# Kernel optimization log

Hardware: AMD Instinct MI355X
Metric: run time of the kernel (lower is better)

The kernel has to match this reference:

```python
import jax, jax.numpy as jnp
import numpy as np

N_NODES = 100000
N_EDGES = 3200000
N_FEAT = 128
DIM = 256
N_CLASSES = 16
BN_EPS = 1e-5


def _glorot(key, shape):
    fan_in, fan_out = shape[0], shape[1]
    lim = float(np.sqrt(6.0 / (fan_in + fan_out)))
    return jax.random.uniform(key, shape, jnp.float32, -lim, lim)


def setup_inputs() -> dict:
    key = jax.random.key(0)
    ks = jax.random.split(key, 16)
    x = jax.random.normal(ks[0], (N_NODES, N_FEAT), jnp.float32)
    edge_index = jax.random.randint(ks[1], (2, N_EDGES), 0, N_NODES, jnp.int64)
    inp = {"x": x, "edge_index": edge_index}
    # conv1 MLP: num_features -> dim -> dim
    inp["w1a"] = _glorot(ks[2], (N_FEAT, DIM)); inp["b1a"] = jnp.zeros((DIM,), jnp.float32)
    inp["w1b"] = _glorot(ks[3], (DIM, DIM));    inp["b1b"] = jnp.zeros((DIM,), jnp.float32)
    inp["g1"] = jnp.ones((DIM,), jnp.float32);  inp["be1"] = jnp.zeros((DIM,), jnp.float32)
    # conv2 MLP
    inp["w2a"] = _glorot(ks[4], (DIM, DIM)); inp["b2a"] = jnp.zeros((DIM,), jnp.float32)
    inp["w2b"] = _glorot(ks[5], (DIM, DIM)); inp["b2b"] = jnp.zeros((DIM,), jnp.float32)
    inp["g2"] = jnp.ones((DIM,), jnp.float32); inp["be2"] = jnp.zeros((DIM,), jnp.float32)
    # conv3 MLP
    inp["w3a"] = _glorot(ks[6], (DIM, DIM)); inp["b3a"] = jnp.zeros((DIM,), jnp.float32)
    inp["w3b"] = _glorot(ks[7], (DIM, DIM)); inp["b3b"] = jnp.zeros((DIM,), jnp.float32)
    # fc2: dim -> num_classes
    inp["wfc"] = _glorot(ks[8], (DIM, N_CLASSES)); inp["bfc"] = jnp.zeros((N_CLASSES,), jnp.float32)
    return inp


def _gin_conv(h, src, dst, wa, ba, wb, bb):
    # sum-aggregate neighbor features: agg[i] = sum_{(j->i)} h[j]; eps=0 so root weight = 1
    agg = jax.ops.segment_sum(h[src], dst, num_segments=N_NODES)
    z = jax.nn.relu((h + agg) @ wa + ba)
    return z @ wb + bb


def _batchnorm(h, gamma, beta):
    # training-mode BN over node dim (biased variance, as torch forward)
    m = h.mean(axis=0)
    v = ((h - m) ** 2).mean(axis=0)
    return gamma * (h - m) / jnp.sqrt(v + BN_EPS) + beta


def reference(x, edge_index, w1a, b1a, w1b, b1b, g1, be1,
              w2a, b2a, w2b, b2b, g2, be2,
              w3a, b3a, w3b, b3b, wfc, bfc):
    src, dst = edge_index[0], edge_index[1]
    h = jax.nn.relu(_gin_conv(x, src, dst, w1a, b1a, w1b, b1b))
    h = _batchnorm(h, g1, be1)
    h = jax.nn.relu(_gin_conv(h, src, dst, w2a, b2a, w2b, b2b))
    h = _batchnorm(h, g2, be2)
    h = jax.nn.relu(_gin_conv(h, src, dst, w3a, b3a, w3b, b3b))
    # dropout p=0.5 is identity in eval mode
    logits = h @ wfc + bfc
    return jax.nn.log_softmax(logits, axis=-1)
```

## Files before the change

### kernel.cpp

```cpp
#include <hip/hip_runtime.h>

typedef unsigned int  u32;
typedef unsigned short u16;

#define NND 100000
#define MPAD 100096
#define NE  3200000
#define F0  128
#define DIM 256
#define NC  16

#define BSH   9
#define NBUCK 196
#define CAP   18432
#define EPB   8192

typedef __bf16 bf16x8 __attribute__((ext_vector_type(8)));
typedef float  f32x4  __attribute__((ext_vector_type(4)));

__device__ __forceinline__ float b2f(u16 h){ return __uint_as_float(((u32)h)<<16); }
__device__ __forceinline__ u16 f2b(float f){
    u32 u = __float_as_uint(f);
    return (u16)((u + 0x7fffu + ((u>>16)&1u)) >> 16);
}
__device__ __forceinline__ float lo16(u32 u){ return __uint_as_float(u<<16); }
__device__ __forceinline__ float hi16(u32 u){ return __uint_as_float(u & 0xffff0000u); }

__device__ __forceinline__ void gload16(const u16* g, u16* l){
    __builtin_amdgcn_global_load_lds(
        (const __attribute__((address_space(1))) u32*)g,
        (__attribute__((address_space(3))) u32*)l, 16, 0, 0);
}

__global__ void probe_kernel(const u32* __restrict__ xw, const int* __restrict__ ei,
                             int* __restrict__ mode, int* __restrict__ gcur,
                             float* __restrict__ stats){
    int t = threadIdx.x;
    if(t < NBUCK) gcur[t] = 0;
    #pragma unroll
    for(int i=0;i<4;i++) stats[t + 256*i] = 0.f;
    if(t==0){
        int insane = 0;
        for(int i=0;i<64;i++){
            u32 w  = xw[i];
            u32 lo = w & 0xffffu;
            u32 e  = (lo >> 7) & 0xff;
            if(lo != 0 && (e < 48 || e > 208)) insane++;
        }
        mode[0] = (insane > 8) ? 1 : 0;
        int zeros = 0;
        for(int i=0;i<16;i++) if(ei[2*i+1]==0) zeros++;
        mode[1] = (zeros==16) ? 1 : 0;
    }
}

__device__ __forceinline__ int ld_src(const int* ei, int i64f, long e){
    return i64f ? ei[2*e] : ei[e];
}
__device__ __forceinline__ int ld_dst(const int* ei, int i64f, long e){
    return i64f ? ei[2*((long)NE + e)] : ei[(long)NE + e];
}

__global__ __launch_bounds__(256) void bucketA(const int* __restrict__ ei,
        const int* __restrict__ mode, u32* __restrict__ bucketArr,
        int* __restrict__ gcur){
    __shared__ u32 stag[EPB];
    __shared__ u16 sbuck[EPB];
    __shared__ int cnt[NBUCK];
    __shared__ int ofs[NBUCK];
    __shared__ int wofs[NBUCK];
    __shared__ int gbase[NBUCK];
    __shared__ int ps[256];
    int tid = threadIdx.x;
    int i64f = mode[1];
    long e0 = (long)blockIdx.x * EPB;
    int n = (int)min((long)EPB, (long)NE - e0);
    if(tid < NBUCK) cnt[tid] = 0;
    __syncthreads();
    for(int i=tid;i<n;i+=256){
        int d = ld_dst(ei, i64f, e0+i);
        atomicAdd(&cnt[d>>BSH], 1);
    }
    __syncthreads();
    ps[tid] = (tid < NBUCK) ? cnt[tid] : 0;
    __syncthreads();
    for(int o=1;o<256;o<<=1){
        int v = (tid>=o) ? ps[tid-o] : 0;
        __syncthreads();
        ps[tid] += v;
        __syncthreads();
    }
    if(tid < NBUCK){
        int ex = ps[tid] - cnt[tid];
        ofs[tid] = ex; wofs[tid] = ex;
        gbase[tid] = cnt[tid] ? atomicAdd(&gcur[tid], cnt[tid]) : 0;
    }
    __syncthreads();
    for(int i=tid;i<n;i+=256){
        int s = ld_src(ei, i64f, e0+i);
        int d = ld_dst(ei, i64f, e0+i);
        int b = d>>BSH;
        int r = atomicAdd(&wofs[b], 1);
        stag[r]  = ((u32)s<<BSH) | (u32)(d & ((1<<BSH)-1));
        sbuck[r] = (u16)b;
    }
    __syncthreads();
    for(int i=tid;i<n;i+=256){
        int b = sbuck[i];
        int pos = gbase[b] + (i - ofs[b]);
        if(pos < CAP) bucketArr[(size_t)b*CAP + pos] = stag[i];
    }
}

__global__ __launch_bounds__(256) void bucketB(const u32* __restrict__ bucketArr,
        const int* __restrict__ gcnt,
        int* __restrict__ rp, int* __restrict__ ssrc){
    __shared__ u32 stag[CAP];
    __shared__ int deg[512];
    __shared__ int lrp[512];
    __shared__ int cur[512];
    __shared__ int ps[256];
    int b = blockIdx.x, tid = threadIdx.x;
    ps[tid] = (tid < NBUCK) ? gcnt[tid] : 0;
    __syncthreads();
    for(int o=1;o<256;o<<=1){
        int v = (tid>=o) ? ps[tid-o] : 0;
        __syncthreads();
        ps[tid] += v;
        __syncthreads();
    }
    int base = (b>0) ? ps[b-1] : 0;
    int n = min(gcnt[b], CAP);
    const u32* ba = bucketArr + (size_t)b*CAP;
    deg[tid] = 0; deg[tid+256] = 0;
    __syncthreads();
    for(int i=tid;i<n;i+=256){
        atomicAdd(&deg[ba[i] & 511], 1);
    }
    __syncthreads();
    ps[tid] = deg[2*tid] + deg[2*tid+1];
    __syncthreads();
    for(int o=1;o<256;o<<=1){
        int v = (tid>=o) ? ps[tid-o] : 0;
        __syncthreads();
        ps[tid] += v;
        __syncthreads();
    }
    {
        int ep = (tid==0) ? 0 : ps[tid-1];
        lrp[2*tid]   = ep;
        lrp[2*tid+1] = ep + deg[2*tid];
        cur[2*tid]   = lrp[2*tid];
        cur[2*tid+1] = lrp[2*tid+1];
    }
    __syncthreads();
    for(int i=tid;i<512;i+=256){
        int node = (b<<BSH) + i;
        if(node <= NND) rp[node] = base + lrp[i];
    }
    for(int i=tid;i<n;i+=256){
        u32 v = ba[i];
        int r = atomicAdd(&cur[v & 511], 1);
        stag[r] = v >> BSH;
    }
    __syncthreads();
    for(int i=tid;i<n;i+=256){
        ssrc[base + i] = (int)stag[i];
    }
}

__global__ void cvt_x(const float* __restrict__ xf, u16* __restrict__ Xc,
                      const int* __restrict__ mode){
    if(!mode[0]) return;
    size_t i = ((size_t)blockIdx.x*256 + threadIdx.x)*8;
    float4 a = *(const float4*)(xf+i);
    float4 b = *(const float4*)(xf+i+4);
    uint4 pk;
    pk.x = (u32)f2b(a.x) | ((u32)f2b(a.y)<<16);
    pk.y = (u32)f2b(a.z) | ((u32)f2b(a.w)<<16);
    pk.z = (u32)f2b(b.x) | ((u32)f2b(b.y)<<16);
    pk.w = (u32)f2b(b.z) | ((u32)f2b(b.w)<<16);
    *(uint4*)(Xc + i) = pk;
}

__device__ __forceinline__ float ldf(const void* p, int i, int f32f){
    return f32f ? ((const float*)p)[i] : b2f(((const u16*)p)[i]);
}
__global__ void merged_cvt(
        const void* w1a, const void* w1b, const void* w2a, const void* w2b,
        const void* w3a, const void* w3b, const void* wfc,
        const void* b1a, const void* b1b, const void* g1, const void* be1,
        const void* b2a, const void* b2b, const void* g2, const void* be2,
        const void* b3a, const void* b3b, const void* bfcp,
        u16* __restrict__ Wt1a, u16* __restrict__ Wt1b, u16* __restrict__ Wt2a,
        u16* __restrict__ Wt2b, u16* __restrict__ Wt3a, u16* __restrict__ Wt3b,
        u16* __restrict__ Wfc, u16* __restrict__ Vc, const int* __restrict__ mode){
    int b = blockIdx.x, t = threadIdx.x;
    int f32f = mode[0];
    if(b < 128){
        int id = b*256 + t;
        int k = id / DIM, n = id % DIM;
        Wt1a[n*F0 + k] = f2b(ldf(w1a, id, f32f));
        return;
    }
    b -= 128;
    if(b < 5*256){
        int wi = b >> 8;
        const void* W = (wi==0)?w1b:(wi==1)?w2a:(wi==2)?w2b:(wi==3)?w3a:w3b;
        u16* Wt = (wi==0)?Wt1b:(wi==1)?Wt2a:(wi==2)?Wt2b:(wi==3)?Wt3a:Wt3b;
        int id = (b & 255)*256 + t;
        int k = id / DIM, n = id % DIM;
        Wt[n*DIM + k] = f2b(ldf(W, id, f32f));
        return;
    }
    b -= 5*256;
    if(b < 16){
        int id = b*256 + t;
        int k = id / NC, c = id % NC;
        Wfc[c*DIM + k] = f2b(ldf(wfc, id, f32f));
        return;
    }
    b -= 16;
    {
        const void* ps[11] = {b1a,b1b,g1,be1,b2a,b2b,g2,be2,b3a,b3b,bfcp};
        int lens[11] = {DIM,DIM,DIM,DIM,DIM,DIM,DIM,DIM,DIM,DIM,NC};
        if(t < lens[b]) Vc[b*256 + t] = f2b(ldf(ps[b], t, f32f));
    }
}

template<int LPI>
__global__ __launch_bounds__(256) void agg2(const u16* __restrict__ hA,
        const u16* __restrict__ hB, const int* __restrict__ mode,
        const int* __restrict__ rp, const int* __restrict__ ssrc,
        u16* __restrict__ out,
        const float* __restrict__ stats, const u16* __restrict__ g,
        const u16* __restrict__ be, int use_bn, int M){
    const int F = LPI*8;
    const int IPW = 64/LPI;
    int node = blockIdx.x*4 + (threadIdx.x>>6);
    if(node >= M) return;
    int lane = threadIdx.x & 63;
    int li   = lane & (LPI-1);
    int slot = lane / LPI;
    const u16* h = (LPI==16 && mode[0]) ? hB : hA;
    const int boff = li*8;

    int e0 = rp[node], e1 = rp[node+1];
    int n_items = e1 - e0 + 1;
    float acc[8] = {0.f,0.f,0.f,0.f,0.f,0.f,0.f,0.f};

    auto item = [&](int i)->int { return (i==0) ? node : ssrc[e0 + i - 1]; };
    auto addu = [&](uint4 u){
        acc[0]+=lo16(u.x); acc[1]+=hi16(u.x);
        acc[2]+=lo16(u.y); acc[3]+=hi16(u.y);
        acc[4]+=lo16(u.z); acc[5]+=hi16(u.z);
        acc[6]+=lo16(u.w); acc[7]+=hi16(u.w);
    };

    int i = 0;
    for(; i + 4*IPW <= n_items; i += 4*IPW){
        int s0 = item(i + slot);
        int s1 = item(i + IPW + slot);
        int s2 = item(i + 2*IPW + slot);
        int s3 = item(i + 3*IPW + slot);
        uint4 u0 = *(const uint4*)(h + (size_t)s0*F + boff);
        uint4 u1 = *(const uint4*)(h + (size_t)s1*F + boff);
        uint4 u2 = *(const uint4*)(h + (size_t)s2*F + boff);
        uint4 u3 = *(const uint4*)(h + (size_t)s3*F + boff);
        addu(u0); addu(u1); addu(u2); addu(u3);
    }
    for(; i + IPW <= n_items; i += IPW){
        int s = item(i + slot);
        addu(*(const uint4*)(h + (size_t)s*F + boff));
    }
    if(i < n_items){
        int r = n_items - i;
        if(slot < r){
            int s = item(i + slot);
            addu(*(const uint4*)(h + (size_t)s*F + boff));
        }
    }

    #pragma unroll
    for(int j=0;j<8;j++){
        if(LPI==16) acc[j] += __shfl_xor(acc[j], 16);
        acc[j] += __shfl_xor(acc[j], 32);
    }

    if(slot == 0){
        float res[8];
        if(use_bn){
            float inv_m = 1.0f / (float)M;
            float cnt = (float)n_items;
            #pragma unroll
            for(int j=0;j<8;j++){
                int f = boff + j;
                float mean = stats[f]*inv_m;
                float var  = fmaxf(stats[F+f]*inv_m - mean*mean, 0.f);
                float rstd = rsqrtf(var + 1e-5f);
                float gg = b2f(g[f]);
                float a = gg*rstd;
                float bb = b2f(be[f]) - a*mean;
                res[j] = a*acc[j] + cnt*bb;
            }
        } else {
            #pragma unroll
            for(int j=0;j<8;j++) res[j] = acc[j];
        }
        uint4 o;
        o.x = (u32)f2b(res[0]) | ((u32)f2b(res[1])<<16);
        o.y = (u32)f2b(res[2]) | ((u32)f2b(res[3])<<16);
        o.z = (u32)f2b(res[4]) | ((u32)f2b(res[5])<<16);
        o.w = (u32)f2b(res[6]) | ((u32)f2b(res[7])<<16);
        *(uint4*)(out + (size_t)node*F + boff) = o;
    }
}

#define TBM 128
#define TBN 128
#define TBK 32
__global__ __launch_bounds__(256) void gemm128(
        const u16* __restrict__ A, const u16* __restrict__ Bt,
        const u16* __restrict__ bias, u16* __restrict__ C,
        int N, int K, int do_relu, float* __restrict__ stats, int do_stats){
    __shared__ __align__(16) u16 lA[TBM*TBK];
    __shared__ __align__(16) u16 lB[TBN*TBK];
    __shared__ float colS[TBN], colS2[TBN];
    int tid = threadIdx.x;
    int w = tid>>6, lane = tid&63;
    int q = lane>>4, mr = lane&15;
    int wr = w>>1, wc = w&1;
    int m0 = blockIdx.x*TBM, n0 = blockIdx.y*TBN;

    if(do_stats){
        if(tid < TBN){ colS[tid]=0.f; colS2[tid]=0.f; }
    }

    f32x4 acc[4][4];
    #pragma unroll
    for(int i=0;i<4;i++)
        #pragma unroll
        for(int c=0;c<4;c++) acc[i][c] = (f32x4){0.f,0.f,0.f,0.f};

    const u16* ga0 = A  + (size_t)(m0 + w*32 + (lane>>2))*K + (lane&3)*8;
    const u16* ga1 = ga0 + (size_t)16*K;
    const u16* gb0 = Bt + (size_t)(n0 + w*32 + (lane>>2))*K + (lane&3)*8;
    const u16* gb1 = gb0 + (size_t)16*K;
    u16* la0 = &lA[(w*32)*TBK];    u16* la1 = la0 + 16*TBK;
    u16* lb0 = &lB[(w*32)*TBK];    u16* lb1 = lb0 + 16*TBK;

    for(int k0=0; k0<K; k0+=TBK){
        gload16(ga0, la0); gload16(ga1, la1);
        gload16(gb0, lb0); gload16(gb1, lb1);
        ga0 += TBK; ga1 += TBK; gb0 += TBK; gb1 += TBK;
        __syncthreads();
        bf16x8 af[4], bfr[4];
        #pragma unroll
        for(int i=0;i<4;i++)
            af[i] = *reinterpret_cast<const bf16x8*>(&lA[(wr*64 + i*16 + mr)*TBK + q*8]);
        #pragma unroll
        for(int c=0;c<4;c++)
            bfr[c] = *reinterpret_cast<const bf16x8*>(&lB[(wc*64 + c*16 + mr)*TBK + q*8]);
        #pragma unroll
        for(int i=0;i<4;i++)
            #pragma unroll
            for(int c=0;c<4;c++)
                acc[i][c] = __builtin_amdgcn_mfma_f32_16x16x32_bf16(af[i], bfr[c], acc[i][c], 0, 0, 0);
        __syncthreads();
    }

    #pragma unroll
    for(int c=0;c<4;c++){
        int lcol = wc*64 + c*16 + mr;
        int col  = n0 + lcol;
        float bv = b2f(bias[col]);
        float s = 0.f, s2 = 0.f;
        #pragma unroll
        for(int i=0;i<4;i++){
            int row = m0 + wr*64 + i*16 + q*4;
            #pragma unroll
            for(int r=0;r<4;r++){
                float v = acc[i][c][r] + bv;
                if(do_relu) v = fmaxf(v, 0.f);
                u16 o = f2b(v);
                C[(size_t)(row + r)*N + col] = o;
                if(do_stats && (row + r) < NND){
                    float vr = b2f(o);
                    s += vr; s2 += vr*vr;
                }
            }
        }
        if(do_stats){
            atomicAdd(&colS[lcol], s);
            atomicAdd(&colS2[lcol], s2);
        }
    }
    if(do_stats){
        __syncthreads();
        if(tid < TBN){
            int col = n0 + tid;
            atomicAdd(&stats[col], colS[tid]);
            atomicAdd(&stats[DIM+col], colS2[tid]);
        }
    }
}

__global__ __launch_bounds__(256) void fc_lsm(const u16* __restrict__ h,
        const u16* __restrict__ wfcT, const u16* __restrict__ bfc,
        void* __restrict__ out, const int* __restrict__ mode, int M){
    __shared__ float lds[256];
    __shared__ float rmx[16], rls[16];
    int tid = threadIdx.x;
    int r = tid>>4, c = tid&15;
    int row = blockIdx.x*16 + r;
    float acc = b2f(bfc[c]);
    const u16* hp = h + (size_t)row*DIM;
    const u16* wp = wfcT + c*DIM;
    for(int k=0;k<DIM;k+=8){
        uint4 hv = *(const uint4*)(hp+k);
        uint4 wv = *(const uint4*)(wp+k);
        acc += lo16(hv.x)*lo16(wv.x) + hi16(hv.x)*hi16(wv.x)
             + lo16(hv.y)*lo16(wv.y) + hi16(hv.y)*hi16(wv.y)
             + lo16(hv.z)*lo16(wv.z) + hi16(hv.z)*hi16(wv.z)
             + lo16(hv.w)*lo16(wv.w) + hi16(hv.w)*hi16(wv.w);
    }
    lds[tid] = acc;
    __syncthreads();
    if(c==0){
        float mx = -1e30f;
        for(int i=0;i<NC;i++) mx = fmaxf(mx, lds[r*NC+i]);
        float s = 0.f;
        for(int i=0;i<NC;i++) s += expf(lds[r*NC+i] - mx);
        rmx[r] = mx; rls[r] = logf(s);
    }
    __syncthreads();
    if(row < M){
        float v = acc - rmx[r] - rls[r];
        if(mode[0]) ((float*)out)[(size_t)row*NC + c] = v;
        else        ((u16*)out)[(size_t)row*NC + c] = f2b(v);
    }
}

extern "C" void kernel_launch(void* const* d_in, const int* in_sizes, int n_in,
                              void* d_out, int out_size, void* d_ws, size_t ws_size,
                              hipStream_t stream){
    const void* x   = d_in[0];
    const int*  ei  = (const int*)d_in[1];
    const void* w1a = d_in[2];  const void* b1a = d_in[3];
    const void* w1b = d_in[4];  const void* b1b = d_in[5];
    const void* g1  = d_in[6];  const void* be1 = d_in[7];
    const void* w2a = d_in[8];  const void* b2a = d_in[9];
    const void* w2b = d_in[10]; const void* b2b = d_in[11];
    const void* g2  = d_in[12]; const void* be2 = d_in[13];
    const void* w3a = d_in[14]; const void* b3a = d_in[15];
    const void* w3b = d_in[16]; const void* b3b = d_in[17];
    const void* wfc = d_in[18]; const void* bfc = d_in[19];

    char* base = (char*)d_ws;
    size_t off = 0;
    auto alloc = [&](size_t bytes)->void*{
        void* p = base + off;
        off = (off + bytes + 255) & ~(size_t)255;
        return p;
    };
    u16*  P     = (u16*)alloc((size_t)MPAD*DIM*2);
    u16*  Q     = (u16*)alloc((size_t)MPAD*DIM*2);
    int*  ssrc  = (int*)alloc((size_t)NE*4);
    u32*  bArr  = (u32*)alloc((size_t)NBUCK*CAP*4);
    int*  gcur  = (int*)alloc((size_t)NBUCK*4);
    int*  rp    = (int*)alloc((size_t)(NND+1)*4);
    float* stats= (float*)alloc(4*DIM*4);
    int*  mode  = (int*)alloc(16);
    u16* Wt1a = (u16*)alloc((size_t)F0*DIM*2);
    u16* Wt1b = (u16*)alloc((size_t)DIM*DIM*2);
    u16* Wt2a = (u16*)alloc((size_t)DIM*DIM*2);
    u16* Wt2b = (u16*)alloc((size_t)DIM*DIM*2);
    u16* Wt3a = (u16*)alloc((size_t)DIM*DIM*2);
    u16* Wt3b = (u16*)alloc((size_t)DIM*DIM*2);
    u16* Vc   = (u16*)alloc(11*256*2);
    u16* Wfc  = (u16*)alloc((size_t)DIM*NC*2);
    u16* Xc   = P;
    float* statsA = stats;
    float* statsB = stats + 2*DIM;

    probe_kernel<<<1, 256, 0, stream>>>((const u32*)x, ei, mode, gcur, stats);

    bucketA<<<(NE + EPB - 1)/EPB, 256, 0, stream>>>(ei, mode, bArr, gcur);
    bucketB<<<NBUCK, 256, 0, stream>>>(bArr, gcur, rp, ssrc);

    cvt_x<<<(NND*F0)/(256*8), 256, 0, stream>>>((const float*)x, Xc, mode);
    merged_cvt<<<128 + 5*256 + 16 + 11, 256, 0, stream>>>(
        w1a,w1b,w2a,w2b,w3a,w3b,wfc, b1a,b1b,g1,be1,b2a,b2b,g2,be2,b3a,b3b,bfc,
        Wt1a,Wt1b,Wt2a,Wt2b,Wt3a,Wt3b,Wfc,Vc, mode);

    dim3 ggrid(MPAD/TBM, DIM/TBN);

    agg2<16><<<NND/4, 256, 0, stream>>>((const u16*)x, Xc, mode, rp, ssrc, Q,
                                        statsA, Vc, Vc, 0, NND);
    gemm128<<<ggrid, 256, 0, stream>>>(Q, Wt1a, Vc+0*256, P, DIM, F0, 1, statsA, 0);
    gemm128<<<ggrid, 256, 0, stream>>>(P, Wt1b, Vc+1*256, Q, DIM, DIM, 1, statsA, 1);

    agg2<32><<<NND/4, 256, 0, stream>>>(Q, Q, mode, rp, ssrc, P,
                                        statsA, Vc+2*256, Vc+3*256, 1, NND);
    gemm128<<<ggrid, 256, 0, stream>>>(P, Wt2a, Vc+4*256, Q, DIM, DIM, 1, statsB, 0);
    gemm128<<<ggrid, 256, 0, stream>>>(Q, Wt2b, Vc+5*256, P, DIM, DIM, 1, statsB, 1);

    agg2<32><<<NND/4, 256, 0, stream>>>(P, P, mode, rp, ssrc, Q,
                                        statsB, Vc+6*256, Vc+7*256, 1, NND);
    gemm128<<<ggrid, 256, 0, stream>>>(Q, Wt3a, Vc+8*256, P, DIM, DIM, 1, statsA, 0);
    gemm128<<<ggrid, 256, 0, stream>>>(P, Wt3b, Vc+9*256, Q, DIM, DIM, 1, statsA, 0);

    fc_lsm<<<NND/16, 256, 0, stream>>>(Q, Wfc, Vc+10*256, d_out, mode, NND);
}
```

Baseline: 1.153 ms.

## Fuse two-layer MLP GEMMs per GIN conv and deepen gather unroll

Each GIN conv's two GEMMs are merged into one kernel. Every block computes a 64-row tile of the full 256-wide first layer, keeps the ReLU'd intermediate in LDS, and runs the second GEMM from there. This removes the intermediate round trip through global memory and one launch per layer. In exchange, every block reloads both full weight matrices and LDS use rises, which may cut occupancy. The aggregation gather loop is also unrolled from 4 to 8 loads in flight to raise memory-level parallelism.

```diff
diff --git a/kernel.cpp b/kernel.cpp
--- a/kernel.cpp
+++ b/kernel.cpp
@@ -258,16 +258,15 @@
     };
 
     int i = 0;
-    for(; i + 4*IPW <= n_items; i += 4*IPW){
-        int s0 = item(i + slot);
-        int s1 = item(i + IPW + slot);
-        int s2 = item(i + 2*IPW + slot);
-        int s3 = item(i + 3*IPW + slot);
-        uint4 u0 = *(const uint4*)(h + (size_t)s0*F + boff);
-        uint4 u1 = *(const uint4*)(h + (size_t)s1*F + boff);
-        uint4 u2 = *(const uint4*)(h + (size_t)s2*F + boff);
-        uint4 u3 = *(const uint4*)(h + (size_t)s3*F + boff);
-        addu(u0); addu(u1); addu(u2); addu(u3);
+    for(; i + 8*IPW <= n_items; i += 8*IPW){
+        int s[8];
+        #pragma unroll
+        for(int j=0;j<8;j++) s[j] = item(i + j*IPW + slot);
+        uint4 u[8];
+        #pragma unroll
+        for(int j=0;j<8;j++) u[j] = *(const uint4*)(h + (size_t)s[j]*F + boff);
+        #pragma unroll
+        for(int j=0;j<8;j++) addu(u[j]);
     }
     for(; i + IPW <= n_items; i += IPW){
         int s = item(i + slot);
@@ -316,25 +315,24 @@
     }
 }
 
-#define TBM 128
-#define TBN 128
-#define TBK 32
-__global__ __launch_bounds__(256) void gemm128(
-        const u16* __restrict__ A, const u16* __restrict__ Bt,
-        const u16* __restrict__ bias, u16* __restrict__ C,
-        int N, int K, int do_relu, float* __restrict__ stats, int do_stats){
-    __shared__ __align__(16) u16 lA[TBM*TBK];
-    __shared__ __align__(16) u16 lB[TBN*TBK];
-    __shared__ float colS[TBN], colS2[TBN];
+#define FBM 64
+#define FBK 32
+#define ZP  264
+__global__ __launch_bounds__(256) void mlp_fused(
+        const u16* __restrict__ A, const u16* __restrict__ WaT,
+        const u16* __restrict__ ba, const u16* __restrict__ WbT,
+        const u16* __restrict__ bb, u16* __restrict__ C,
+        int Ka, float* __restrict__ stats, int do_stats){
+    __shared__ __align__(16) u16 lA[FBM*FBK];
+    __shared__ __align__(16) u16 lB[DIM*FBK];
+    __shared__ __align__(16) u16 zt[FBM*ZP];
+    __shared__ float colS[DIM], colS2[DIM];
     int tid = threadIdx.x;
     int w = tid>>6, lane = tid&63;
     int q = lane>>4, mr = lane&15;
-    int wr = w>>1, wc = w&1;
-    int m0 = blockIdx.x*TBM, n0 = blockIdx.y*TBN;
-
-    if(do_stats){
-        if(tid < TBN){ colS[tid]=0.f; colS2[tid]=0.f; }
-    }
+    int m0 = blockIdx.x*FBM;
+
+    if(do_stats){ colS[tid]=0.f; colS2[tid]=0.f; }
 
     f32x4 acc[4][4];
     #pragma unroll
@@ -342,48 +340,83 @@
         #pragma unroll
         for(int c=0;c<4;c++) acc[i][c] = (f32x4){0.f,0.f,0.f,0.f};
 
-    const u16* ga0 = A  + (size_t)(m0 + w*32 + (lane>>2))*K + (lane&3)*8;
-    const u16* ga1 = ga0 + (size_t)16*K;
-    const u16* gb0 = Bt + (size_t)(n0 + w*32 + (lane>>2))*K + (lane&3)*8;
-    const u16* gb1 = gb0 + (size_t)16*K;
-    u16* la0 = &lA[(w*32)*TBK];    u16* la1 = la0 + 16*TBK;
-    u16* lb0 = &lB[(w*32)*TBK];    u16* lb1 = lb0 + 16*TBK;
-
-    for(int k0=0; k0<K; k0+=TBK){
-        gload16(ga0, la0); gload16(ga1, la1);
-        gload16(gb0, lb0); gload16(gb1, lb1);
-        ga0 += TBK; ga1 += TBK; gb0 += TBK; gb1 += TBK;
-        __syncthreads();
-        bf16x8 af[4], bfr[4];
-        #pragma unroll
-        for(int i=0;i<4;i++)
-            af[i] = *reinterpret_cast<const bf16x8*>(&lA[(wr*64 + i*16 + mr)*TBK + q*8]);
-        #pragma unroll
-        for(int c=0;c<4;c++)
-            bfr[c] = *reinterpret_cast<const bf16x8*>(&lB[(wc*64 + c*16 + mr)*TBK + q*8]);
-        #pragma unroll
-        for(int i=0;i<4;i++)
+    {
+        const u16* gA = A + (size_t)(m0 + (tid>>2))*Ka + (tid&3)*8;
+        u16* lAd = &lA[tid*16/2];
+        for(int k0=0; k0<Ka; k0+=FBK){
+            gload16(gA, lAd); gA += FBK;
+            #pragma unroll
+            for(int j=0;j<4;j++){
+                int s = j*256 + tid;
+                gload16(WaT + (size_t)(s>>2)*Ka + k0 + (s&3)*8, &lB[s*8]);
+            }
+            __syncthreads();
+            bf16x8 af[4], bf[4];
+            #pragma unroll
+            for(int i=0;i<4;i++)
+                af[i] = *reinterpret_cast<const bf16x8*>(&lA[(i*16+mr)*FBK + q*8]);
             #pragma unroll
             for(int c=0;c<4;c++)
-                acc[i][c] = __builtin_amdgcn_mfma_f32_16x16x32_bf16(af[i], bfr[c], acc[i][c], 0, 0, 0);
-        __syncthreads();
-    }
-
+                bf[c] = *reinterpret_cast<const bf16x8*>(&lB[(w*64+c*16+mr)*FBK + q*8]);
+            #pragma unroll
+            for(int i=0;i<4;i++)
+                #pragma unroll
+                for(int c=0;c<4;c++)
+                    acc[i][c] = __builtin_amdgcn_mfma_f32_16x16x32_bf16(af[i], bf[c], acc[i][c], 0, 0, 0);
+            __syncthreads();
+        }
+    }
     #pragma unroll
     for(int c=0;c<4;c++){
-        int lcol = wc*64 + c*16 + mr;
-        int col  = n0 + lcol;
-        float bv = b2f(bias[col]);
+        int col = w*64 + c*16 + mr;
+        float bav = b2f(ba[col]);
+        #pragma unroll
+        for(int i=0;i<4;i++){
+            #pragma unroll
+            for(int r=0;r<4;r++){
+                int row = i*16 + q*4 + r;
+                zt[row*ZP + col] = f2b(fmaxf(acc[i][c][r] + bav, 0.f));
+            }
+            acc[i][c] = (f32x4){0.f,0.f,0.f,0.f};
+        }
+    }
+    __syncthreads();
+
+    for(int k0=0; k0<DIM; k0+=FBK){
+        #pragma unroll
+        for(int j=0;j<4;j++){
+            int s = j*256 + tid;
+            gload16(WbT + (size_t)(s>>2)*DIM + k0 + (s&3)*8, &lB[s*8]);
+        }
+        __syncthreads();
+        bf16x8 af[4], bf[4];
+        #pragma unroll
+        for(int i=0;i<4;i++)
+            af[i] = *reinterpret_cast<const bf16x8*>(&zt[(i*16+mr)*ZP + k0 + q*8]);
+        #pragma unroll
+        for(int c=0;c<4;c++)
+            bf[c] = *reinterpret_cast<const bf16x8*>(&lB[(w*64+c*16+mr)*FBK + q*8]);
+        #pragma unroll
+        for(int i=0;i<4;i++)
+            #pragma unroll
+            for(int c=0;c<4;c++)
+                acc[i][c] = __builtin_amdgcn_mfma_f32_16x16x32_bf16(af[i], bf[c], acc[i][c], 0, 0, 0);
+        __syncthreads();
+    }
+
+    #pragma unroll
+    for(int c=0;c<4;c++){
+        int col = w*64 + c*16 + mr;
+        float bv = b2f(bb[col]);
         float s = 0.f, s2 = 0.f;
         #pragma unroll
         for(int i=0;i<4;i++){
-            int row = m0 + wr*64 + i*16 + q*4;
+            int row = m0 + i*16 + q*4;
             #pragma unroll
             for(int r=0;r<4;r++){
-                float v = acc[i][c][r] + bv;
-                if(do_relu) v = fmaxf(v, 0.f);
+                float v = fmaxf(acc[i][c][r] + bv, 0.f);
                 u16 o = f2b(v);
-                C[(size_t)(row + r)*N + col] = o;
+                C[(size_t)(row + r)*DIM + col] = o;
                 if(do_stats && (row + r) < NND){
                     float vr = b2f(o);
                     s += vr; s2 += vr*vr;
@@ -391,17 +424,14 @@
             }
         }
         if(do_stats){
-            atomicAdd(&colS[lcol], s);
-            atomicAdd(&colS2[lcol], s2);
+            atomicAdd(&colS[col], s);
+            atomicAdd(&colS2[col], s2);
         }
     }
     if(do_stats){
         __syncthreads();
-        if(tid < TBN){
-            int col = n0 + tid;
-            atomicAdd(&stats[col], colS[tid]);
-            atomicAdd(&stats[DIM+col], colS2[tid]);
-        }
+        atomicAdd(&stats[tid], colS[tid]);
+        atomicAdd(&stats[DIM+tid], colS2[tid]);
     }
 }
 
@@ -493,22 +523,22 @@
         w1a,w1b,w2a,w2b,w3a,w3b,wfc, b1a,b1b,g1,be1,b2a,b2b,g2,be2,b3a,b3b,bfc,
         Wt1a,Wt1b,Wt2a,Wt2b,Wt3a,Wt3b,Wfc,Vc, mode);
 
-    dim3 ggrid(MPAD/TBM, DIM/TBN);
+    int mgrid = MPAD/FBM;
 
     agg2<16><<<NND/4, 256, 0, stream>>>((const u16*)x, Xc, mode, rp, ssrc, Q,
                                         statsA, Vc, Vc, 0, NND);
-    gemm128<<<ggrid, 256, 0, stream>>>(Q, Wt1a, Vc+0*256, P, DIM, F0, 1, statsA, 0);
-    gemm128<<<ggrid, 256, 0, stream>>>(P, Wt1b, Vc+1*256, Q, DIM, DIM, 1, statsA, 1);
-
-    agg2<32><<<NND/4, 256, 0, stream>>>(Q, Q, mode, rp, ssrc, P,
+    mlp_fused<<<mgrid, 256, 0, stream>>>(Q, Wt1a, Vc+0*256, Wt1b, Vc+1*256, P,
+                                         F0, statsA, 1);
+
+    agg2<32><<<NND/4, 256, 0, stream>>>(P, P, mode, rp, ssrc, Q,
                                         statsA, Vc+2*256, Vc+3*256, 1, NND);
-    gemm128<<<ggrid, 256, 0, stream>>>(P, Wt2a, Vc+4*256, Q, DIM, DIM, 1, statsB, 0);
-    gemm128<<<ggrid, 256, 0, stream>>>(Q, Wt2b, Vc+5*256, P, DIM, DIM, 1, statsB, 1);
+    mlp_fused<<<mgrid, 256, 0, stream>>>(Q, Wt2a, Vc+4*256, Wt2b, Vc+5*256, P,
+                                         DIM, statsB, 1);
 
     agg2<32><<<NND/4, 256, 0, stream>>>(P, P, mode, rp, ssrc, Q,
                                         statsB, Vc+6*256, Vc+7*256, 1, NND);
-    gemm128<<<ggrid, 256, 0, stream>>>(Q, Wt3a, Vc+8*256, P, DIM, DIM, 1, statsA, 0);
-    gemm128<<<ggrid, 256, 0, stream>>>(P, Wt3b, Vc+9*256, Q, DIM, DIM, 1, statsA, 0);
-
-    fc_lsm<<<NND/16, 256, 0, stream>>>(Q, Wfc, Vc+10*256, d_out, mode, NND);
-}
+    mlp_fused<<<mgrid, 256, 0, stream>>>(Q, Wt3a, Vc+8*256, Wt3b, Vc+9*256, P,
+                                         DIM, statsA, 0);
+
+    fc_lsm<<<NND/16, 256, 0, stream>>>(P, Wfc, Vc+10*256, d_out, mode, NND);
+}
```

New measurement: 1.110 ms. 1.04x faster.
